# Kernel optimization log

Hardware: AMD Instinct MI355X
Metric: run time of the kernel (lower is better)

## Reference

```python
import jax, jax.numpy as jnp
import numpy as np

INPUT_DIM = 3
NUM_LEVELS = 16
LEVEL_DIM = 2
PER_LEVEL_SCALE = 2
BASE_RES = 16
MAX_PARAMS = 2 ** 19
BATCH = 2 ** 21

PRIMES = np.array([1, 2654435761, 805459861], dtype=np.uint32)
SORTED_BIN_MASK = np.triu(np.ones((INPUT_DIM + 1, INPUT_DIM), dtype=np.int32))


def _offsets():
    offs, off = [], 0
    for i in range(NUM_LEVELS):
        res = int(np.ceil(BASE_RES * PER_LEVEL_SCALE ** i))
        p = min(MAX_PARAMS, res ** INPUT_DIM)
        p = int(np.ceil(p / 32) * 32)
        off += p
        offs.append(off)
    return offs

OFFSETS = _offsets()  # cumulative, last entry = total table rows = 7114752


def setup_inputs() -> dict:
    key = jax.random.key(0)
    k1, k2 = jax.random.split(key)
    inputs = jax.random.uniform(k1, (BATCH, INPUT_DIM), dtype=jnp.float32)
    # xavier-uniform-ish init for the hash table
    total = OFFSETS[-1]
    a = float(np.sqrt(6.0 / (total + LEVEL_DIM)))
    embeddings = jax.random.uniform(k2, (total, LEVEL_DIM), dtype=jnp.float32,
                                    minval=-a, maxval=a)
    return {"inputs": inputs, "embeddings": embeddings}


def _fast_hash(ind_u32, hash_size):
    # ind_u32: [..., 3] uint32; uint32 multiply wraps mod 2^32 == (& 0xFFFFFFFF)
    h = ind_u32 * jnp.asarray(PRIMES)
    h = h[..., 0] ^ h[..., 1] ^ h[..., 2]
    return h % jnp.uint32(hash_size)


def _forward(inputs, embeddings):
    bin_mask_tbl = jnp.asarray(SORTED_BIN_MASK)  # [d+1, d]
    outs = []
    prev = 0
    for i in range(NUM_LEVELS):
        res = int(np.ceil(BASE_RES * PER_LEVEL_SCALE ** i))
        x = inputs * res                      # [B, d]
        xi = x.astype(jnp.int32)              # trunc == floor for x >= 0
        xf = x - jax.lax.stop_gradient(xi.astype(x.dtype))
        inds = jnp.argsort(xf, axis=-1)
        sorted_xf = jnp.take_along_axis(xf, inds, axis=-1)
        inv_inds = jnp.argsort(inds, axis=-1)
        bin_mask = bin_mask_tbl[:, inv_inds].transpose(1, 0, 2)  # [B, d+1, d]
        neigs = xi[:, None, :] + bin_mask                        # [B, d+1, d]
        hash_size = OFFSETS[i] - prev
        hids = _fast_hash(neigs.astype(jnp.uint32), hash_size).astype(jnp.int32) + prev
        feats = embeddings[hids]              # [B, d+1, level_dim] irregular gather
        # barycentric-style weights: consecutive diffs of sorted fracs padded with 0/1
        w_upper = jnp.concatenate([sorted_xf, jnp.ones_like(sorted_xf[..., :1])], axis=-1)
        w_lower = jnp.concatenate([jnp.zeros_like(sorted_xf[..., :1]), sorted_xf], axis=-1)
        w = (w_upper - w_lower)[..., None]    # [B, d+1, 1]
        outs.append(jnp.sum(feats * w, axis=-2))  # [B, level_dim]
        prev = OFFSETS[i]
    return jnp.concatenate(outs, axis=-1)     # [B, num_levels * level_dim]


def reference(inputs, embeddings):
    return _forward(inputs, embeddings)
```

## Files before the change

kernel.cpp:

```cpp
#include <hip/hip_runtime.h>
#include <stdint.h>


constexpr uint32_t kBatch   = 1u << 21;
constexpr uint32_t kQuarter = kBatch / 4u;
constexpr size_t   kSlab    = (size_t)kBatch * 2u;

typedef float f32x2 __attribute__((ext_vector_type(2)));
typedef float f32x4 __attribute__((ext_vector_type(4)));

constexpr uint32_t PREV[16] = {
    0u, 4096u, 36864u, 299008u, 823296u, 1347584u, 1871872u, 2396160u,
    2920448u, 3444736u, 3969024u, 4493312u, 5017600u, 5541888u, 6066176u, 6590464u};
constexpr uint32_t MASK[16] = {
    4095u, 32767u, 262143u, 524287u, 524287u, 524287u, 524287u, 524287u,
    524287u, 524287u, 524287u, 524287u, 524287u, 524287u, 524287u, 524287u};

__device__ __forceinline__ void corner_hashes_weights(
    float x0, float x1, float x2, float res, uint32_t mask, uint32_t prev,
    uint32_t& g0, uint32_t& g1, uint32_t& g2, uint32_t& g3,
    float& sa, float& sb, float& sc)
{
    const float fx0 = x0 * res;
    const float fx1 = x1 * res;
    const float fx2 = x2 * res;
    const int i0 = (int)fx0;
    const int i1 = (int)fx1;
    const int i2 = (int)fx2;
    const float f0 = fx0 - (float)i0;
    const float f1 = fx1 - (float)i1;
    const float f2 = fx2 - (float)i2;

    const int r0 = (int)(f1 < f0) + (int)(f2 < f0);
    const int r1 = (int)(f0 < f1) + (int)(f2 < f1) + (int)(f0 == f1);
    const int r2 = (int)(f0 < f2) + (int)(f1 < f2) + (int)(f0 == f2) + (int)(f1 == f2);

    sa = fminf(fminf(f0, f1), f2);
    sc = fmaxf(fmaxf(f0, f1), f2);
    sb = __builtin_amdgcn_fmed3f(f0, f1, f2);

    const uint32_t A0 = (uint32_t)i0;
    const uint32_t A1 = A0 + 1u;
    const uint32_t B0 = (uint32_t)i1 * 2654435761u;
    const uint32_t B1 = ((uint32_t)i1 + 1u) * 2654435761u;
    const uint32_t C0 = (uint32_t)i2 * 805459861u;
    const uint32_t C1 = ((uint32_t)i2 + 1u) * 805459861u;

    const uint32_t h0 = A1 ^ B1 ^ C1;
    const uint32_t h1 = (r0 >= 1 ? A1 : A0) ^ (r1 >= 1 ? B1 : B0) ^ (r2 >= 1 ? C1 : C0);
    const uint32_t h2 = (r0 >= 2 ? A1 : A0) ^ (r1 >= 2 ? B1 : B0) ^ (r2 >= 2 ? C1 : C0);
    const uint32_t h3 = A0 ^ B0 ^ C0;

    g0 = (h0 & mask) + prev;
    g1 = (h1 & mask) + prev;
    g2 = (h2 & mask) + prev;
    g3 = (h3 & mask) + prev;
}


__global__ __launch_bounds__(256) void gather8(
    const float* __restrict__ in,
    const float* __restrict__ emb,
    float* __restrict__ scr,
    uint32_t base)
{
    const uint32_t bid  = blockIdx.x;
    const uint32_t lvl  = base + (bid >> 11);
    const uint32_t blk  = bid & 2047u;
    const uint32_t tid  = blk * 256u + threadIdx.x;

    const float res = (float)(16u << lvl);
    const uint32_t mask = MASK[lvl];
    const uint32_t prev = PREV[lvl];
    float* slab = scr + (size_t)(lvl - base) * kSlab;

    f32x2 e[4][4];
    float sa[4], sb[4], sc[4];

#pragma unroll
    for (int k = 0; k < 4; ++k) {
        const uint32_t b = tid + (uint32_t)k * kQuarter;
        const float x0 = __builtin_nontemporal_load(in + 3u * b + 0u);
        const float x1 = __builtin_nontemporal_load(in + 3u * b + 1u);
        const float x2 = __builtin_nontemporal_load(in + 3u * b + 2u);
        uint32_t g0, g1, g2, g3;
        corner_hashes_weights(x0, x1, x2, res, mask, prev, g0, g1, g2, g3,
                              sa[k], sb[k], sc[k]);
        e[k][0] = *reinterpret_cast<const f32x2*>(emb + 2u * g0);
        e[k][1] = *reinterpret_cast<const f32x2*>(emb + 2u * g1);
        e[k][2] = *reinterpret_cast<const f32x2*>(emb + 2u * g2);
        e[k][3] = *reinterpret_cast<const f32x2*>(emb + 2u * g3);
    }

    asm volatile(""
        : "+v"(e[0][0]), "+v"(e[0][1]), "+v"(e[0][2]), "+v"(e[0][3]),
          "+v"(e[1][0]), "+v"(e[1][1]), "+v"(e[1][2]), "+v"(e[1][3]),
          "+v"(e[2][0]), "+v"(e[2][1]), "+v"(e[2][2]), "+v"(e[2][3]),
          "+v"(e[3][0]), "+v"(e[3][1]), "+v"(e[3][2]), "+v"(e[3][3]));

#pragma unroll
    for (int k = 0; k < 4; ++k) {
        const float w0 = sa[k];
        const float w1 = sb[k] - sa[k];
        const float w2 = sc[k] - sb[k];
        const float w3 = 1.0f - sc[k];
        f32x2 v;
        v.x = w0 * e[k][0].x + w1 * e[k][1].x + w2 * e[k][2].x + w3 * e[k][3].x;
        v.y = w0 * e[k][0].y + w1 * e[k][1].y + w2 * e[k][2].y + w3 * e[k][3].y;
        const uint32_t b = tid + (uint32_t)k * kQuarter;
        __builtin_nontemporal_store(v, reinterpret_cast<f32x2*>(slab + 2u * (size_t)b));
    }
}

__global__ __launch_bounds__(256) void transpose8(
    const float* __restrict__ scr,
    float* __restrict__ out,
    uint32_t half)
{
    const uint32_t b = blockIdx.x * 256u + threadIdx.x;
    float v[16];
#pragma unroll
    for (int l = 0; l < 8; ++l) {
        const f32x2 e = __builtin_nontemporal_load(
            reinterpret_cast<const f32x2*>(scr + (size_t)l * kSlab + 2u * (size_t)b));
        v[2 * l + 0] = e.x;
        v[2 * l + 1] = e.y;
    }
    float* o = out + (size_t)b * 32u + (size_t)half * 16u;
#pragma unroll
    for (int q = 0; q < 4; ++q) {
        f32x4 t;
        t.x = v[4 * q + 0];
        t.y = v[4 * q + 1];
        t.z = v[4 * q + 2];
        t.w = v[4 * q + 3];
        *reinterpret_cast<f32x4*>(o + 4 * q) = t;
    }
}


__global__ __launch_bounds__(256) void pyramid_fwd_mono(
    const float* __restrict__ in,
    const float* __restrict__ emb,
    float* __restrict__ out)
{
    const uint32_t b = blockIdx.x * 256u + threadIdx.x;
    const float x0 = in[3u * b + 0u];
    const float x1 = in[3u * b + 1u];
    const float x2 = in[3u * b + 2u];

#pragma unroll
    for (int g = 0; g < 2; ++g) {
        float o8[16];
#pragma unroll
        for (int k = 0; k < 8; ++k) {
            const int lvl = g * 8 + k;
            const float res = (float)(16 << lvl);
            uint32_t g0, g1, g2, g3;
            float sa, sb, sc;
            corner_hashes_weights(x0, x1, x2, res, MASK[lvl], PREV[lvl],
                                  g0, g1, g2, g3, sa, sb, sc);
            const f32x2 e0 = *reinterpret_cast<const f32x2*>(emb + 2u * g0);
            const f32x2 e1 = *reinterpret_cast<const f32x2*>(emb + 2u * g1);
            const f32x2 e2 = *reinterpret_cast<const f32x2*>(emb + 2u * g2);
            const f32x2 e3 = *reinterpret_cast<const f32x2*>(emb + 2u * g3);
            const float w0 = sa, w1 = sb - sa, w2 = sc - sb, w3 = 1.0f - sc;
            o8[2 * k + 0] = w0 * e0.x + w1 * e1.x + w2 * e2.x + w3 * e3.x;
            o8[2 * k + 1] = w0 * e0.y + w1 * e1.y + w2 * e2.y + w3 * e3.y;
        }
        f32x4* o = reinterpret_cast<f32x4*>(out + (size_t)b * 32u + (size_t)g * 16u);
#pragma unroll
        for (int q = 0; q < 4; ++q) {
            f32x4 v;
            v.x = o8[4 * q + 0];
            v.y = o8[4 * q + 1];
            v.z = o8[4 * q + 2];
            v.w = o8[4 * q + 3];
            o[q] = v;
        }
    }
}


extern "C" void kernel_launch(void* const* d_in, const int* in_sizes, int n_in,
                              void* d_out, int out_size, void* d_ws, size_t ws_size,
                              hipStream_t stream) {
    const float* in  = (const float*)d_in[0];
    const float* emb = (const float*)d_in[1];
    float* out = (float*)d_out;

    const size_t need = (size_t)8 * kSlab * sizeof(float);
    if (ws_size >= need) {
        float* scr = (float*)d_ws;
        dim3 gg(8u * 2048u), tb(256u), gt(kBatch / 256u);
        hipLaunchKernelGGL(gather8, gg, tb, 0, stream, in, emb, scr, 0u);
        hipLaunchKernelGGL(transpose8, gt, tb, 0, stream, scr, out, 0u);
        hipLaunchKernelGGL(gather8, gg, tb, 0, stream, in, emb, scr, 8u);
        hipLaunchKernelGGL(transpose8, gt, tb, 0, stream, scr, out, 1u);
    } else {
        dim3 grid(kBatch / 256u), block(256u);
        hipLaunchKernelGGL(pyramid_fwd_mono, grid, block, 0, stream, in, emb, out);
    }
}
```

Before: 726.1 us.

## Make gather kernel loop over levels with fewer blocks and 8 points per thread

```diff
diff --git a/kernel.cpp b/kernel.cpp
--- a/kernel.cpp
+++ b/kernel.cpp
@@ -2,17 +2,19 @@
 #include <stdint.h>
 
 
-constexpr uint32_t kBatch   = 1u << 21;
-constexpr uint32_t kQuarter = kBatch / 4u;
-constexpr size_t   kSlab    = (size_t)kBatch * 2u;
+constexpr uint32_t kBatch  = 1u << 21;
+constexpr uint32_t kGBlks  = 1024u;
+constexpr uint32_t kThr    = 256u;
+constexpr uint32_t kStride = kGBlks * kThr;
+constexpr size_t   kSlab   = (size_t)kBatch * 2u;
 
 typedef float f32x2 __attribute__((ext_vector_type(2)));
 typedef float f32x4 __attribute__((ext_vector_type(4)));
 
-constexpr uint32_t PREV[16] = {
+__constant__ constexpr uint32_t PREV[16] = {
     0u, 4096u, 36864u, 299008u, 823296u, 1347584u, 1871872u, 2396160u,
     2920448u, 3444736u, 3969024u, 4493312u, 5017600u, 5541888u, 6066176u, 6590464u};
-constexpr uint32_t MASK[16] = {
+__constant__ constexpr uint32_t MASK[16] = {
     4095u, 32767u, 262143u, 524287u, 524287u, 524287u, 524287u, 524287u,
     524287u, 524287u, 524287u, 524287u, 524287u, 524287u, 524287u, 524287u};
 
@@ -58,57 +60,63 @@
 }
 
 
-__global__ __launch_bounds__(256) void gather8(
+__global__ __launch_bounds__(256, 4) void gather8(
     const float* __restrict__ in,
     const float* __restrict__ emb,
     float* __restrict__ scr,
     uint32_t base)
 {
-    const uint32_t bid  = blockIdx.x;
-    const uint32_t lvl  = base + (bid >> 11);
-    const uint32_t blk  = bid & 2047u;
-    const uint32_t tid  = blk * 256u + threadIdx.x;
-
-    const float res = (float)(16u << lvl);
-    const uint32_t mask = MASK[lvl];
-    const uint32_t prev = PREV[lvl];
-    float* slab = scr + (size_t)(lvl - base) * kSlab;
-
-    f32x2 e[4][4];
-    float sa[4], sb[4], sc[4];
-
-#pragma unroll
-    for (int k = 0; k < 4; ++k) {
-        const uint32_t b = tid + (uint32_t)k * kQuarter;
-        const float x0 = __builtin_nontemporal_load(in + 3u * b + 0u);
-        const float x1 = __builtin_nontemporal_load(in + 3u * b + 1u);
-        const float x2 = __builtin_nontemporal_load(in + 3u * b + 2u);
-        uint32_t g0, g1, g2, g3;
-        corner_hashes_weights(x0, x1, x2, res, mask, prev, g0, g1, g2, g3,
-                              sa[k], sb[k], sc[k]);
-        e[k][0] = *reinterpret_cast<const f32x2*>(emb + 2u * g0);
-        e[k][1] = *reinterpret_cast<const f32x2*>(emb + 2u * g1);
-        e[k][2] = *reinterpret_cast<const f32x2*>(emb + 2u * g2);
-        e[k][3] = *reinterpret_cast<const f32x2*>(emb + 2u * g3);
-    }
-
-    asm volatile(""
-        : "+v"(e[0][0]), "+v"(e[0][1]), "+v"(e[0][2]), "+v"(e[0][3]),
-          "+v"(e[1][0]), "+v"(e[1][1]), "+v"(e[1][2]), "+v"(e[1][3]),
-          "+v"(e[2][0]), "+v"(e[2][1]), "+v"(e[2][2]), "+v"(e[2][3]),
-          "+v"(e[3][0]), "+v"(e[3][1]), "+v"(e[3][2]), "+v"(e[3][3]));
-
-#pragma unroll
-    for (int k = 0; k < 4; ++k) {
-        const float w0 = sa[k];
-        const float w1 = sb[k] - sa[k];
-        const float w2 = sc[k] - sb[k];
-        const float w3 = 1.0f - sc[k];
-        f32x2 v;
-        v.x = w0 * e[k][0].x + w1 * e[k][1].x + w2 * e[k][2].x + w3 * e[k][3].x;
-        v.y = w0 * e[k][0].y + w1 * e[k][1].y + w2 * e[k][2].y + w3 * e[k][3].y;
-        const uint32_t b = tid + (uint32_t)k * kQuarter;
-        __builtin_nontemporal_store(v, reinterpret_cast<f32x2*>(slab + 2u * (size_t)b));
+    const uint32_t tid = blockIdx.x * kThr + threadIdx.x;
+
+#pragma unroll 1
+    for (uint32_t l8 = 0u; l8 < 8u; ++l8) {
+        const uint32_t lvl = base + l8;
+        const float res = (float)(16u << lvl);
+        const uint32_t mask = MASK[lvl];
+        const uint32_t prev = PREV[lvl];
+        float* slab = scr + (size_t)l8 * kSlab;
+
+        f32x2 e[8][4];
+        float sa[8], sb[8], sc[8];
+
+#pragma unroll
+        for (int k = 0; k < 8; ++k) {
+            const uint32_t b = tid + (uint32_t)k * kStride;
+            const float x0 = __builtin_nontemporal_load(in + 3u * b + 0u);
+            const float x1 = __builtin_nontemporal_load(in + 3u * b + 1u);
+            const float x2 = __builtin_nontemporal_load(in + 3u * b + 2u);
+            uint32_t g0, g1, g2, g3;
+            corner_hashes_weights(x0, x1, x2, res, mask, prev, g0, g1, g2, g3,
+                                  sa[k], sb[k], sc[k]);
+            e[k][0] = *reinterpret_cast<const f32x2*>(emb + 2u * g0);
+            e[k][1] = *reinterpret_cast<const f32x2*>(emb + 2u * g1);
+            e[k][2] = *reinterpret_cast<const f32x2*>(emb + 2u * g2);
+            e[k][3] = *reinterpret_cast<const f32x2*>(emb + 2u * g3);
+        }
+
+        asm volatile(""
+            : "+v"(e[0][0]), "+v"(e[0][1]), "+v"(e[0][2]), "+v"(e[0][3]),
+              "+v"(e[1][0]), "+v"(e[1][1]), "+v"(e[1][2]), "+v"(e[1][3]),
+              "+v"(e[2][0]), "+v"(e[2][1]), "+v"(e[2][2]), "+v"(e[2][3]),
+              "+v"(e[3][0]), "+v"(e[3][1]), "+v"(e[3][2]), "+v"(e[3][3]));
+        asm volatile(""
+            : "+v"(e[4][0]), "+v"(e[4][1]), "+v"(e[4][2]), "+v"(e[4][3]),
+              "+v"(e[5][0]), "+v"(e[5][1]), "+v"(e[5][2]), "+v"(e[5][3]),
+              "+v"(e[6][0]), "+v"(e[6][1]), "+v"(e[6][2]), "+v"(e[6][3]),
+              "+v"(e[7][0]), "+v"(e[7][1]), "+v"(e[7][2]), "+v"(e[7][3]));
+
+#pragma unroll
+        for (int k = 0; k < 8; ++k) {
+            const float w0 = sa[k];
+            const float w1 = sb[k] - sa[k];
+            const float w2 = sc[k] - sb[k];
+            const float w3 = 1.0f - sc[k];
+            f32x2 v;
+            v.x = w0 * e[k][0].x + w1 * e[k][1].x + w2 * e[k][2].x + w3 * e[k][3].x;
+            v.y = w0 * e[k][0].y + w1 * e[k][1].y + w2 * e[k][2].y + w3 * e[k][3].y;
+            const uint32_t b = tid + (uint32_t)k * kStride;
+            __builtin_nontemporal_store(v, reinterpret_cast<f32x2*>(slab + 2u * (size_t)b));
+        }
     }
 }
 
@@ -192,7 +200,7 @@
     const size_t need = (size_t)8 * kSlab * sizeof(float);
     if (ws_size >= need) {
         float* scr = (float*)d_ws;
-        dim3 gg(8u * 2048u), tb(256u), gt(kBatch / 256u);
+        dim3 gg(kGBlks), tb(kThr), gt(kBatch / 256u);
         hipLaunchKernelGGL(gather8, gg, tb, 0, stream, in, emb, scr, 0u);
         hipLaunchKernelGGL(transpose8, gt, tb, 0, stream, scr, out, 0u);
         hipLaunchKernelGGL(gather8, gg, tb, 0, stream, in, emb, scr, 8u);
```

New measurement: 1.028 ms. 1.42x slower.

## Store per-level intermediates as packed fp16 and transpose all levels once

Applied to the files above, without the earlier changes.

```diff
diff --git a/kernel.cpp b/kernel.cpp
--- a/kernel.cpp
+++ b/kernel.cpp
@@ -1,10 +1,11 @@
 #include <hip/hip_runtime.h>
+#include <hip/hip_fp16.h>
 #include <stdint.h>
 
 
 constexpr uint32_t kBatch   = 1u << 21;
 constexpr uint32_t kQuarter = kBatch / 4u;
-constexpr size_t   kSlab    = (size_t)kBatch * 2u;
+constexpr size_t   kWsNeed  = (size_t)kBatch * 16u * sizeof(uint32_t);
 
 typedef float f32x2 __attribute__((ext_vector_type(2)));
 typedef float f32x4 __attribute__((ext_vector_type(4)));
@@ -57,11 +58,17 @@
     g3 = (h3 & mask) + prev;
 }
 
+__device__ __forceinline__ uint32_t pack_f16x2(float x, float y) {
+    const __half hx = __float2half(x);
+    const __half hy = __float2half(y);
+    return (uint32_t)__half_as_ushort(hx) | ((uint32_t)__half_as_ushort(hy) << 16);
+}
+
 
 __global__ __launch_bounds__(256) void gather8(
     const float* __restrict__ in,
     const float* __restrict__ emb,
-    float* __restrict__ scr,
+    uint32_t* __restrict__ scr,
     uint32_t base)
 {
     const uint32_t bid  = blockIdx.x;
@@ -72,7 +79,7 @@
     const float res = (float)(16u << lvl);
     const uint32_t mask = MASK[lvl];
     const uint32_t prev = PREV[lvl];
-    float* slab = scr + (size_t)(lvl - base) * kSlab;
+    uint32_t* slab = scr + (size_t)lvl * kBatch;
 
     f32x2 e[4][4];
     float sa[4], sb[4], sc[4];
@@ -104,36 +111,32 @@
         const float w1 = sb[k] - sa[k];
         const float w2 = sc[k] - sb[k];
         const float w3 = 1.0f - sc[k];
-        f32x2 v;
-        v.x = w0 * e[k][0].x + w1 * e[k][1].x + w2 * e[k][2].x + w3 * e[k][3].x;
-        v.y = w0 * e[k][0].y + w1 * e[k][1].y + w2 * e[k][2].y + w3 * e[k][3].y;
+        const float vx = w0 * e[k][0].x + w1 * e[k][1].x + w2 * e[k][2].x + w3 * e[k][3].x;
+        const float vy = w0 * e[k][0].y + w1 * e[k][1].y + w2 * e[k][2].y + w3 * e[k][3].y;
         const uint32_t b = tid + (uint32_t)k * kQuarter;
-        __builtin_nontemporal_store(v, reinterpret_cast<f32x2*>(slab + 2u * (size_t)b));
-    }
-}
-
-__global__ __launch_bounds__(256) void transpose8(
-    const float* __restrict__ scr,
-    float* __restrict__ out,
-    uint32_t half)
+        __builtin_nontemporal_store(pack_f16x2(vx, vy), slab + b);
+    }
+}
+
+__global__ __launch_bounds__(256) void transpose16(
+    const uint32_t* __restrict__ scr,
+    float* __restrict__ out)
 {
     const uint32_t b = blockIdx.x * 256u + threadIdx.x;
-    float v[16];
-#pragma unroll
-    for (int l = 0; l < 8; ++l) {
-        const f32x2 e = __builtin_nontemporal_load(
-            reinterpret_cast<const f32x2*>(scr + (size_t)l * kSlab + 2u * (size_t)b));
-        v[2 * l + 0] = e.x;
-        v[2 * l + 1] = e.y;
-    }
-    float* o = out + (size_t)b * 32u + (size_t)half * 16u;
-#pragma unroll
-    for (int q = 0; q < 4; ++q) {
+
+    uint32_t p[16];
+#pragma unroll
+    for (int l = 0; l < 16; ++l)
+        p[l] = __builtin_nontemporal_load(scr + (size_t)l * kBatch + b);
+
+    float* o = out + (size_t)b * 32u;
+#pragma unroll
+    for (int q = 0; q < 8; ++q) {
         f32x4 t;
-        t.x = v[4 * q + 0];
-        t.y = v[4 * q + 1];
-        t.z = v[4 * q + 2];
-        t.w = v[4 * q + 3];
+        t.x = __half2float(__ushort_as_half((unsigned short)(p[2 * q + 0] & 0xFFFFu)));
+        t.y = __half2float(__ushort_as_half((unsigned short)(p[2 * q + 0] >> 16)));
+        t.z = __half2float(__ushort_as_half((unsigned short)(p[2 * q + 1] & 0xFFFFu)));
+        t.w = __half2float(__ushort_as_half((unsigned short)(p[2 * q + 1] >> 16)));
         *reinterpret_cast<f32x4*>(o + 4 * q) = t;
     }
 }
@@ -189,16 +192,17 @@
     const float* emb = (const float*)d_in[1];
     float* out = (float*)d_out;
 
-    const size_t need = (size_t)8 * kSlab * sizeof(float);
-    if (ws_size >= need) {
-        float* scr = (float*)d_ws;
-        dim3 gg(8u * 2048u), tb(256u), gt(kBatch / 256u);
+    dim3 tb(256u);
+
+    if (ws_size >= kWsNeed) {
+        uint32_t* scr = (uint32_t*)d_ws;
+        dim3 gg(8u * 2048u);
+        dim3 gt(kBatch / 256u);
         hipLaunchKernelGGL(gather8, gg, tb, 0, stream, in, emb, scr, 0u);
-        hipLaunchKernelGGL(transpose8, gt, tb, 0, stream, scr, out, 0u);
         hipLaunchKernelGGL(gather8, gg, tb, 0, stream, in, emb, scr, 8u);
-        hipLaunchKernelGGL(transpose8, gt, tb, 0, stream, scr, out, 1u);
+        hipLaunchKernelGGL(transpose16, gt, tb, 0, stream, scr, out);
     } else {
-        dim3 grid(kBatch / 256u), block(256u);
-        hipLaunchKernelGGL(pyramid_fwd_mono, grid, block, 0, stream, in, emb, out);
-    }
-}
+        dim3 grid(kBatch / 256u);
+        hipLaunchKernelGGL(pyramid_fwd_mono, grid, tb, 0, stream, in, emb, out);
+    }
+}
```

Measured after the change: 685.3 us. 5.6% less time.
